# Performance work log

Measured on AMD Instinct MI355X. Metric: run time of the kernel, lower is better.

## Reference

```python
import jax, jax.numpy as jnp
import numpy as np

N_NODES = 100000
DROPOUT_P = 0.2


def _gcn_conv(x, W, b, src, dst, n_nodes):
    # PyG GCNConv: h = x @ W; add self-loops; sym-norm deg^-1/2 aggregation; + bias
    h = x @ W  # [N, D_out]
    loops = jnp.arange(n_nodes, dtype=src.dtype)
    src_all = jnp.concatenate([src, loops])
    dst_all = jnp.concatenate([dst, loops])
    deg = jax.ops.segment_sum(jnp.ones_like(dst_all, dtype=h.dtype), dst_all,
                              num_segments=n_nodes)  # includes self-loops
    dinv = jnp.where(deg > 0, jax.lax.rsqrt(deg), 0.0)
    norm = dinv[src_all] * dinv[dst_all]  # [E+N]
    msg = h[src_all] * norm[:, None]      # gather + scale
    out = jax.ops.segment_sum(msg, dst_all, num_segments=n_nodes)  # scatter-add
    return out + b


def setup_inputs() -> dict:
    key = jax.random.key(0)
    k1, k2, k3, k4 = jax.random.split(key, 4)
    x = jax.random.normal(k1, (N_NODES, 128), dtype=jnp.float32)
    edge_index = jax.random.randint(k2, (2, 1600000), 0, N_NODES, dtype=jnp.int64)
    W1 = jax.random.normal(k3, (128, 64), dtype=jnp.float32) * (1.0 / np.sqrt(128))
    b1 = jnp.zeros((64,), dtype=jnp.float32)
    W2 = jax.random.normal(k4, (64, 32), dtype=jnp.float32) * (1.0 / np.sqrt(64))
    b2 = jnp.zeros((32,), dtype=jnp.float32)
    return {"x": x, "edge_index": edge_index, "W1": W1, "b1": b1, "W2": W2, "b2": b2}


def reference(x, edge_index, W1, b1, W2, b2):
    src, dst = edge_index[0], edge_index[1]
    h1 = _gcn_conv(x, W1, b1, src, dst, N_NODES)
    h1 = jax.nn.relu(h1)
    # F.dropout defaults to training=True -> apply inverted dropout with fixed key
    keep = jax.random.bernoulli(jax.random.key(42), 1.0 - DROPOUT_P, h1.shape)
    h1 = jnp.where(keep, h1 / (1.0 - DROPOUT_P), 0.0)
    h2 = _gcn_conv(h1, W2, b2, src, dst, N_NODES)
    return h2
```

## Files before the change

kernel.cpp:

```cpp
#include <hip/hip_runtime.h>
#include <stdint.h>

#define DIN 128
#define D1 64
#define D2 32
#define MAXDEG 48
#define BCAP 4608
#define CBLK 2048

__device__ __forceinline__ unsigned short f2bf(float v) {
  unsigned u = __float_as_uint(v);
  unsigned r = u + 0x7fffu + ((u >> 16) & 1u);
  return (unsigned short)(r >> 16);
}
__device__ __forceinline__ float bflo(unsigned u) { return __uint_as_float(u << 16); }
__device__ __forceinline__ float bfhi(unsigned u) { return __uint_as_float(u & 0xffff0000u); }

__device__ __forceinline__ unsigned rotl32(unsigned x, int r) {
  return (x << r) | (x >> (32 - r));
}

__device__ __forceinline__ unsigned threefry_fold(unsigned ctr) {
  unsigned k0 = 0u, k1 = 42u;
  unsigned ks0 = k0, ks1 = k1, ks2 = k0 ^ k1 ^ 0x1BD11BDAu;
  unsigned x0 = 0u, x1 = ctr;
  x0 += ks0; x1 += ks1;
#define TF_ROUND(r) { x0 += x1; x1 = rotl32(x1, (r)); x1 ^= x0; }
  TF_ROUND(13) TF_ROUND(15) TF_ROUND(26) TF_ROUND(6)
  x0 += ks1; x1 += ks2 + 1u;
  TF_ROUND(17) TF_ROUND(29) TF_ROUND(16) TF_ROUND(24)
  x0 += ks2; x1 += ks0 + 2u;
  TF_ROUND(13) TF_ROUND(15) TF_ROUND(26) TF_ROUND(6)
  x0 += ks0; x1 += ks1 + 3u;
  TF_ROUND(17) TF_ROUND(29) TF_ROUND(16) TF_ROUND(24)
  x0 += ks1; x1 += ks2 + 4u;
  TF_ROUND(13) TF_ROUND(15) TF_ROUND(26) TF_ROUND(6)
  x0 += ks2; x1 += ks0 + 5u;
#undef TF_ROUND
  return x0 ^ x1;
}

__device__ __forceinline__ float dropout_scale(unsigned idx) {
  unsigned bits = threefry_fold(idx);
  float u = __uint_as_float((bits >> 9) | 0x3f800000u) - 1.0f;
  return (u < 0.8f) ? 1.25f : 0.0f;
}

__device__ __forceinline__ uint4 grow64(const unsigned short* p, int s, int fc) {
  return *(const uint4*)((const char*)p + (((unsigned)s << 7) + ((unsigned)fc << 1)));
}
__device__ __forceinline__ uint4 grow32(const unsigned short* p, int s, int fc) {
  return *(const uint4*)((const char*)p + (((unsigned)s << 6) + ((unsigned)fc << 1)));
}

__device__ __forceinline__ void addpk(float2& a, unsigned u) {
  a.x += bflo(u);
  a.y += bfhi(u);
}
__device__ __forceinline__ void addpkm(float2& a, unsigned u, float m) {
  a.x = fmaf(m, bflo(u), a.x);
  a.y = fmaf(m, bfhi(u), a.y);
}

__global__ __launch_bounds__(256) void bin_kernel(const int* __restrict__ src,
                                                  const int* __restrict__ dst,
                                                  int* __restrict__ cursor,
                                                  uint2* __restrict__ binned,
                                                  int E, int NBK) {
  __shared__ int cnt[512];
  __shared__ int cbase[512];
  const int tid = threadIdx.x;
  const int e0 = blockIdx.x * CBLK;

  for (int b = tid; b < NBK; b += 256) cnt[b] = 0;
  __syncthreads();

#pragma unroll
  for (int i = 0; i < CBLK / 256; i++) {
    int e = e0 + tid + 256 * i;
    if (e < E) atomicAdd(&cnt[dst[e] >> 8], 1);
  }
  __syncthreads();

  for (int b = tid; b < NBK; b += 256) {
    int c = cnt[b];
    if (c > 0) cbase[b] = b * BCAP + atomicAdd(&cursor[b], c);
    cnt[b] = 0;
  }
  __syncthreads();

#pragma unroll
  for (int i = 0; i < CBLK / 256; i++) {
    int e = e0 + tid + 256 * i;
    if (e < E) {
      int d = dst[e];
      int b = d >> 8;
      int rk = atomicAdd(&cnt[b], 1);
      int pos = cbase[b] + rk;
      if (pos - b * BCAP < BCAP)
        binned[pos] = make_uint2((unsigned)d, (unsigned)src[e]);
    }
  }
}

__global__ __launch_bounds__(256) void ellbuild_kernel(const uint2* __restrict__ binned,
                                                       const int* __restrict__ cursor,
                                                       int* __restrict__ deg,
                                                       float* __restrict__ dinv,
                                                       int* __restrict__ ell, int N) {
  __shared__ int r[256];
  const int tid = threadIdx.x;
  const int b = blockIdx.x;
  const int nodebase = b << 8;
  r[tid] = 0;
  __syncthreads();

  int cnt = cursor[b];
  if (cnt > BCAP) cnt = BCAP;
  const uint2* seg = binned + (size_t)b * BCAP;
  for (int i = tid; i < cnt; i += 256) {
    uint2 p = seg[i];
    int local = (int)p.x - nodebase;
    int rk = atomicAdd(&r[local], 1);
    if (rk < MAXDEG) ell[(int)p.x * MAXDEG + rk] = (int)p.y;
  }
  __syncthreads();

  int node = nodebase + tid;
  if (node < N) {
    int dg = r[tid];
    deg[node] = dg;
    dinv[node] = (float)(1.0 / sqrt((double)(dg + 1)));
  }
}

__global__ __launch_bounds__(256) void gemm1_kernel(const float* __restrict__ x,
                                                    const float* __restrict__ W1,
                                                    const float* __restrict__ dinv,
                                                    unsigned short* __restrict__ h1p, int N) {
  __shared__ float xT[32][65];
  __shared__ float Wl[32][D1];
  const int tid = threadIdx.x;
  const int rowbase = blockIdx.x * 64;
  const int tx = tid & 15;
  const int ty = tid >> 4;
  float acc[4][4];
#pragma unroll
  for (int i = 0; i < 4; i++)
#pragma unroll
    for (int j = 0; j < 4; j++) acc[i][j] = 0.f;

  for (int c4 = 0; c4 < 4; c4++) {
    const int k0 = c4 * 32;
#pragma unroll
    for (int i = 0; i < 2; i++) {
      int f = tid + 256 * i;
      int row = f >> 3;
      int kq = (f & 7) * 4;
      int gr = rowbase + row;
      float4 vv = make_float4(0.f, 0.f, 0.f, 0.f);
      if (gr < N) vv = *(const float4*)(x + (size_t)gr * DIN + k0 + kq);
      xT[kq + 0][row] = vv.x;
      xT[kq + 1][row] = vv.y;
      xT[kq + 2][row] = vv.z;
      xT[kq + 3][row] = vv.w;
    }
#pragma unroll
    for (int i = 0; i < 2; i++) {
      int f = tid + 256 * i;
      int k = f >> 4;
      int cc = (f & 15) * 4;
      *(float4*)&Wl[k][cc] = *(const float4*)(W1 + (size_t)(k0 + k) * D1 + cc);
    }
    __syncthreads();
#pragma unroll 4
    for (int k = 0; k < 32; k++) {
      float4 a = *(const float4*)&xT[k][4 * ty];
      float4 b = *(const float4*)&Wl[k][4 * tx];
      float av[4] = {a.x, a.y, a.z, a.w};
      float bv[4] = {b.x, b.y, b.z, b.w};
#pragma unroll
      for (int i = 0; i < 4; i++)
#pragma unroll
        for (int j = 0; j < 4; j++) acc[i][j] = fmaf(av[i], bv[j], acc[i][j]);
    }
    __syncthreads();
  }

#pragma unroll
  for (int i = 0; i < 4; i++) {
    int gr = rowbase + 4 * ty + i;
    if (gr < N) {
      float di = dinv[gr];
      ushort4 o;
      o.x = f2bf(acc[i][0] * di);
      o.y = f2bf(acc[i][1] * di);
      o.z = f2bf(acc[i][2] * di);
      o.w = f2bf(acc[i][3] * di);
      *(ushort4*)(h1p + (size_t)gr * D1 + 4 * tx) = o;
    }
  }
}

__global__ __launch_bounds__(256) void agg1_kernel(const int* __restrict__ deg,
                                                   const float* __restrict__ dinv,
                                                   const int* __restrict__ ell,
                                                   const unsigned short* __restrict__ h1p,
                                                   const float* __restrict__ b1,
                                                   float* __restrict__ h1d, int N) {
  __shared__ float red[4][528];
  const int wslot = __builtin_amdgcn_readfirstlane(threadIdx.x >> 6);
  const int d = blockIdx.x * 4 + wslot;
  const int lane = threadIdx.x & 63;
  const int eslot = lane >> 3;
  const int fc = (lane & 7) << 3;
  const int cnt = min(deg[d], MAXDEG);
  const int base = d * MAXDEG;

  float2 acc[4];
  {
    uint4 sv = grow64(h1p, d, fc);
    float m = (eslot == 0) ? 1.0f : 0.0f;
    acc[0] = make_float2(m * bflo(sv.x), m * bfhi(sv.x));
    acc[1] = make_float2(m * bflo(sv.y), m * bfhi(sv.y));
    acc[2] = make_float2(m * bflo(sv.z), m * bfhi(sv.z));
    acc[3] = make_float2(m * bflo(sv.w), m * bfhi(sv.w));
  }

  int j = 0;
  for (; j + 16 <= cnt; j += 16) {
    int s0 = ell[base + j + eslot];
    int s1 = ell[base + j + 8 + eslot];
    uint4 v0 = grow64(h1p, s0, fc);
    uint4 v1 = grow64(h1p, s1, fc);
    addpk(acc[0], v0.x); addpk(acc[1], v0.y); addpk(acc[2], v0.z); addpk(acc[3], v0.w);
    addpk(acc[0], v1.x); addpk(acc[1], v1.y); addpk(acc[2], v1.z); addpk(acc[3], v1.w);
  }
  if (j < cnt) {
    int e0 = j + eslot;
    int e1 = e0 + 8;
    int s0 = ell[base + e0];
    int s1 = ell[base + e1];
    s0 = (e0 < cnt) ? s0 : d;
    s1 = (e1 < cnt) ? s1 : d;
    float m0 = (e0 < cnt) ? 1.0f : 0.0f;
    float m1 = (e1 < cnt) ? 1.0f : 0.0f;
    uint4 v0 = grow64(h1p, s0, fc);
    uint4 v1 = grow64(h1p, s1, fc);
    addpkm(acc[0], v0.x, m0); addpkm(acc[1], v0.y, m0); addpkm(acc[2], v0.z, m0); addpkm(acc[3], v0.w, m0);
    addpkm(acc[0], v1.x, m1); addpkm(acc[1], v1.y, m1); addpkm(acc[2], v1.z, m1); addpkm(acc[3], v1.w, m1);
  }

  float* wred = red[wslot];
  *(float4*)&wred[eslot * 66 + fc]     = make_float4(acc[0].x, acc[0].y, acc[1].x, acc[1].y);
  *(float4*)&wred[eslot * 66 + fc + 4] = make_float4(acc[2].x, acc[2].y, acc[3].x, acc[3].y);
  const int f = fc + eslot;
  float v = 0.f;
#pragma unroll
  for (int e = 0; e < 8; e++) v += wred[e * 66 + f];

  float o = fmaf(dinv[d], v, b1[f]);
  o = fmaxf(o, 0.0f);
  o *= dropout_scale((unsigned)(d * D1 + f));
  h1d[(size_t)d * D1 + f] = o;
}

__global__ __launch_bounds__(256) void gemm2_kernel(const float* __restrict__ h1d,
                                                    const float* __restrict__ W2,
                                                    const float* __restrict__ dinv,
                                                    unsigned short* __restrict__ h2p, int N) {
  __shared__ float hT[D1][129];
  __shared__ float Wl[D1][D2];
  const int tid = threadIdx.x;
  const int rowbase = blockIdx.x * 128;

#pragma unroll
  for (int i = 0; i < 8; i++) {
    int f = tid + 256 * i;
    int row = f >> 4;
    int kq = (f & 15) * 4;
    int gr = rowbase + row;
    float4 v = make_float4(0.f, 0.f, 0.f, 0.f);
    if (gr < N) v = *(const float4*)(h1d + (size_t)gr * D1 + kq);
    hT[kq + 0][row] = v.x;
    hT[kq + 1][row] = v.y;
    hT[kq + 2][row] = v.z;
    hT[kq + 3][row] = v.w;
  }
#pragma unroll
  for (int i = 0; i < 2; i++) {
    int f = tid + 256 * i;
    int k = f >> 3;
    int c = (f & 7) * 4;
    *(float4*)&Wl[k][c] = *(const float4*)(W2 + (size_t)k * D2 + c);
  }
  __syncthreads();

  const int tx = tid & 7;
  const int ty = tid >> 3;
  float acc[4][4];
#pragma unroll
  for (int i = 0; i < 4; i++)
#pragma unroll
    for (int j = 0; j < 4; j++) acc[i][j] = 0.f;

#pragma unroll 4
  for (int k = 0; k < D1; k++) {
    float4 a = *(const float4*)&hT[k][4 * ty];
    float4 b = *(const float4*)&Wl[k][4 * tx];
    float av[4] = {a.x, a.y, a.z, a.w};
    float bv[4] = {b.x, b.y, b.z, b.w};
#pragma unroll
    for (int i = 0; i < 4; i++)
#pragma unroll
      for (int j = 0; j < 4; j++) acc[i][j] = fmaf(av[i], bv[j], acc[i][j]);
  }

#pragma unroll
  for (int i = 0; i < 4; i++) {
    int gr = rowbase + 4 * ty + i;
    if (gr < N) {
      float di = dinv[gr];
      ushort4 o;
      o.x = f2bf(acc[i][0] * di);
      o.y = f2bf(acc[i][1] * di);
      o.z = f2bf(acc[i][2] * di);
      o.w = f2bf(acc[i][3] * di);
      *(ushort4*)(h2p + (size_t)gr * D2 + 4 * tx) = o;
    }
  }
}

__global__ __launch_bounds__(256) void agg2_kernel(const int* __restrict__ deg,
                                                   const float* __restrict__ dinv,
                                                   const int* __restrict__ ell,
                                                   const unsigned short* __restrict__ h2p,
                                                   const float* __restrict__ b2,
                                                   float* __restrict__ out, int N) {
  __shared__ float red[4][544];
  const int wslot = __builtin_amdgcn_readfirstlane(threadIdx.x >> 6);
  const int d = blockIdx.x * 4 + wslot;
  const int lane = threadIdx.x & 63;
  const int eslot = lane >> 2;
  const int fc = (lane & 3) << 3;
  const int cnt = min(deg[d], MAXDEG);
  const int base = d * MAXDEG;

  float2 acc[4];
  {
    uint4 sv = grow32(h2p, d, fc);
    float m = (eslot == 0) ? 1.0f : 0.0f;
    acc[0] = make_float2(m * bflo(sv.x), m * bfhi(sv.x));
    acc[1] = make_float2(m * bflo(sv.y), m * bfhi(sv.y));
    acc[2] = make_float2(m * bflo(sv.z), m * bfhi(sv.z));
    acc[3] = make_float2(m * bflo(sv.w), m * bfhi(sv.w));
  }

  int j = 0;
  for (; j + 16 <= cnt; j += 16) {
    int s = ell[base + j + eslot];
    uint4 v = grow32(h2p, s, fc);
    addpk(acc[0], v.x); addpk(acc[1], v.y); addpk(acc[2], v.z); addpk(acc[3], v.w);
  }
  if (j < cnt) {
    int e = j + eslot;
    int s = ell[base + e];
    s = (e < cnt) ? s : d;
    float m = (e < cnt) ? 1.0f : 0.0f;
    uint4 v = grow32(h2p, s, fc);
    addpkm(acc[0], v.x, m); addpkm(acc[1], v.y, m); addpkm(acc[2], v.z, m); addpkm(acc[3], v.w, m);
  }

  float* wred = red[wslot];
  *(float4*)&wred[eslot * 34 + fc]     = make_float4(acc[0].x, acc[0].y, acc[1].x, acc[1].y);
  *(float4*)&wred[eslot * 34 + fc + 4] = make_float4(acc[2].x, acc[2].y, acc[3].x, acc[3].y);
  const int f = fc + (eslot & 7);
  const int ebase = (lane >= 32) ? 8 : 0;
  float v = 0.f;
#pragma unroll
  for (int e = 0; e < 8; e++) v += wred[(ebase + e) * 34 + f];
  v += __shfl_down(v, 32, 64);

  if (lane < 32) {
    out[(size_t)d * D2 + f] = fmaf(dinv[d], v, b2[f]);
  }
}

extern "C" void kernel_launch(void* const* d_in, const int* in_sizes, int n_in,
                              void* d_out, int out_size, void* d_ws, size_t ws_size,
                              hipStream_t stream) {
  const float* x  = (const float*)d_in[0];
  const int*   ei = (const int*)d_in[1];
  const float* W1 = (const float*)d_in[2];
  const float* b1 = (const float*)d_in[3];
  const float* W2 = (const float*)d_in[4];
  const float* b2 = (const float*)d_in[5];
  const int N = in_sizes[0] / DIN;
  const int E = in_sizes[1] / 2;
  const int NBK = (N + 255) >> 8;
  const int* src = ei;
  const int* dst = ei + E;
  float* out = (float*)d_out;

  char* ws = (char*)d_ws;
  size_t off = 0;
  auto alloc = [&](size_t bytes) -> char* {
    char* p = ws + off;
    off += (bytes + 255) / 256 * 256;
    return p;
  };
  unsigned short* h1p = (unsigned short*)alloc((size_t)N * D1 * 2);
  float*          h1d = (float*)alloc((size_t)N * D1 * 4);
  int*            ell = (int*)alloc(((size_t)N * MAXDEG + 64) * 4);
  int*            deg = (int*)alloc((size_t)N * 4);
  float*        dinvp = (float*)alloc((size_t)N * 4);
  int*         cursor = (int*)alloc((size_t)NBK * 4);
  unsigned short* h2p = h1p;
  uint2*       binned = (uint2*)h1d;
  (void)ws_size; (void)n_in; (void)out_size;

  hipMemsetAsync(cursor, 0, (size_t)NBK * 4, stream);

  bin_kernel<<<(E + CBLK - 1) / CBLK, 256, 0, stream>>>(src, dst, cursor, binned, E, NBK);
  ellbuild_kernel<<<NBK, 256, 0, stream>>>(binned, cursor, deg, dinvp, ell, N);
  gemm1_kernel<<<(N + 63) / 64, 256, 0, stream>>>(x, W1, dinvp, h1p, N);
  agg1_kernel<<<N / 4, 256, 0, stream>>>(deg, dinvp, ell, h1p, b1, h1d, N);
  gemm2_kernel<<<(N + 127) / 128, 256, 0, stream>>>(h1d, W2, dinvp, h2p, N);
  agg2_kernel<<<N / 4, 256, 0, stream>>>(deg, dinvp, ell, h2p, b2, out, N);
}
```

Measured before the change: 262.3 us.

## Replace shared-memory binning with sub-bucketed global atomics; fully unroll neighbor gathers

The binning kernel drops the per-block shared-memory histogram and two-pass scatter. Each edge now does a single global atomic into one of 16 sub-buckets per 256-node bucket, chosen by block index to spread contention, and ellbuild walks all 16 sub-buckets. Both aggregation kernels load the whole 48-entry ELL row with one coalesced load per lane and broadcast indices by shuffle. They then issue all gathers up front, fully unrolled and masked, instead of looping. This removes the dependent index loads and exposes more memory parallelism, at the cost of always issuing MAXDEG gathers and more global atomic traffic. Sub-buckets can overflow at SUBCAP 384 more easily than the old single 4608 cap.

```diff
diff --git a/kernel.cpp b/kernel.cpp
--- a/kernel.cpp
+++ b/kernel.cpp
@@ -5,8 +5,8 @@
 #define D1 64
 #define D2 32
 #define MAXDEG 48
-#define BCAP 4608
-#define CBLK 2048
+#define SUBC 16
+#define SUBCAP 384
 
 __device__ __forceinline__ unsigned short f2bf(float v) {
   unsigned u = __float_as_uint(v);
@@ -53,10 +53,6 @@
   return *(const uint4*)((const char*)p + (((unsigned)s << 6) + ((unsigned)fc << 1)));
 }
 
-__device__ __forceinline__ void addpk(float2& a, unsigned u) {
-  a.x += bflo(u);
-  a.y += bfhi(u);
-}
 __device__ __forceinline__ void addpkm(float2& a, unsigned u, float m) {
   a.x = fmaf(m, bflo(u), a.x);
   a.y = fmaf(m, bfhi(u), a.y);
@@ -65,42 +61,15 @@
 __global__ __launch_bounds__(256) void bin_kernel(const int* __restrict__ src,
                                                   const int* __restrict__ dst,
                                                   int* __restrict__ cursor,
-                                                  uint2* __restrict__ binned,
-                                                  int E, int NBK) {
-  __shared__ int cnt[512];
-  __shared__ int cbase[512];
-  const int tid = threadIdx.x;
-  const int e0 = blockIdx.x * CBLK;
-
-  for (int b = tid; b < NBK; b += 256) cnt[b] = 0;
-  __syncthreads();
-
-#pragma unroll
-  for (int i = 0; i < CBLK / 256; i++) {
-    int e = e0 + tid + 256 * i;
-    if (e < E) atomicAdd(&cnt[dst[e] >> 8], 1);
-  }
-  __syncthreads();
-
-  for (int b = tid; b < NBK; b += 256) {
-    int c = cnt[b];
-    if (c > 0) cbase[b] = b * BCAP + atomicAdd(&cursor[b], c);
-    cnt[b] = 0;
-  }
-  __syncthreads();
-
-#pragma unroll
-  for (int i = 0; i < CBLK / 256; i++) {
-    int e = e0 + tid + 256 * i;
-    if (e < E) {
-      int d = dst[e];
-      int b = d >> 8;
-      int rk = atomicAdd(&cnt[b], 1);
-      int pos = cbase[b] + rk;
-      if (pos - b * BCAP < BCAP)
-        binned[pos] = make_uint2((unsigned)d, (unsigned)src[e]);
-    }
-  }
+                                                  uint2* __restrict__ binned, int E) {
+  int e = blockIdx.x * 256 + threadIdx.x;
+  if (e >= E) return;
+  int d = dst[e];
+  int s = src[e];
+  int sub = ((d >> 8) << 4) + (blockIdx.x & (SUBC - 1));
+  int rk = atomicAdd(&cursor[sub], 1);
+  if (rk < SUBCAP)
+    binned[(size_t)sub * SUBCAP + rk] = make_uint2((unsigned)d, (unsigned)s);
 }
 
 __global__ __launch_bounds__(256) void ellbuild_kernel(const uint2* __restrict__ binned,
@@ -115,14 +84,17 @@
   r[tid] = 0;
   __syncthreads();
 
-  int cnt = cursor[b];
-  if (cnt > BCAP) cnt = BCAP;
-  const uint2* seg = binned + (size_t)b * BCAP;
-  for (int i = tid; i < cnt; i += 256) {
-    uint2 p = seg[i];
-    int local = (int)p.x - nodebase;
-    int rk = atomicAdd(&r[local], 1);
-    if (rk < MAXDEG) ell[(int)p.x * MAXDEG + rk] = (int)p.y;
+  for (int k = 0; k < SUBC; k++) {
+    int idx = (b << 4) + k;
+    int cnt = cursor[idx];
+    if (cnt > SUBCAP) cnt = SUBCAP;
+    const uint2* seg = binned + (size_t)idx * SUBCAP;
+    for (int i = tid; i < cnt; i += 256) {
+      uint2 p = seg[i];
+      int local = (int)p.x - nodebase;
+      int rk = atomicAdd(&r[local], 1);
+      if (rk < MAXDEG) ell[(int)p.x * MAXDEG + rk] = (int)p.y;
+    }
   }
   __syncthreads();
 
@@ -217,49 +189,45 @@
   const int cnt = min(deg[d], MAXDEG);
   const int base = d * MAXDEG;
 
+  int sv = ell[base + lane];
+
+  uint4 v[6];
+  float mk[6];
+#pragma unroll
+  for (int seg = 0; seg < 6; seg++) {
+    int e = seg * 8 + eslot;
+    int s = __shfl(sv, e, 64);
+    bool ok = e < cnt;
+    mk[seg] = ok ? 1.0f : 0.0f;
+    v[seg] = grow64(h1p, ok ? s : d, fc);
+  }
+  uint4 self = grow64(h1p, d, fc);
+
   float2 acc[4];
   {
-    uint4 sv = grow64(h1p, d, fc);
     float m = (eslot == 0) ? 1.0f : 0.0f;
-    acc[0] = make_float2(m * bflo(sv.x), m * bfhi(sv.x));
-    acc[1] = make_float2(m * bflo(sv.y), m * bfhi(sv.y));
-    acc[2] = make_float2(m * bflo(sv.z), m * bfhi(sv.z));
-    acc[3] = make_float2(m * bflo(sv.w), m * bfhi(sv.w));
-  }
-
-  int j = 0;
-  for (; j + 16 <= cnt; j += 16) {
-    int s0 = ell[base + j + eslot];
-    int s1 = ell[base + j + 8 + eslot];
-    uint4 v0 = grow64(h1p, s0, fc);
-    uint4 v1 = grow64(h1p, s1, fc);
-    addpk(acc[0], v0.x); addpk(acc[1], v0.y); addpk(acc[2], v0.z); addpk(acc[3], v0.w);
-    addpk(acc[0], v1.x); addpk(acc[1], v1.y); addpk(acc[2], v1.z); addpk(acc[3], v1.w);
-  }
-  if (j < cnt) {
-    int e0 = j + eslot;
-    int e1 = e0 + 8;
-    int s0 = ell[base + e0];
-    int s1 = ell[base + e1];
-    s0 = (e0 < cnt) ? s0 : d;
-    s1 = (e1 < cnt) ? s1 : d;
-    float m0 = (e0 < cnt) ? 1.0f : 0.0f;
-    float m1 = (e1 < cnt) ? 1.0f : 0.0f;
-    uint4 v0 = grow64(h1p, s0, fc);
-    uint4 v1 = grow64(h1p, s1, fc);
-    addpkm(acc[0], v0.x, m0); addpkm(acc[1], v0.y, m0); addpkm(acc[2], v0.z, m0); addpkm(acc[3], v0.w, m0);
-    addpkm(acc[0], v1.x, m1); addpkm(acc[1], v1.y, m1); addpkm(acc[2], v1.z, m1); addpkm(acc[3], v1.w, m1);
+    acc[0] = make_float2(m * bflo(self.x), m * bfhi(self.x));
+    acc[1] = make_float2(m * bflo(self.y), m * bfhi(self.y));
+    acc[2] = make_float2(m * bflo(self.z), m * bfhi(self.z));
+    acc[3] = make_float2(m * bflo(self.w), m * bfhi(self.w));
+  }
+#pragma unroll
+  for (int seg = 0; seg < 6; seg++) {
+    addpkm(acc[0], v[seg].x, mk[seg]);
+    addpkm(acc[1], v[seg].y, mk[seg]);
+    addpkm(acc[2], v[seg].z, mk[seg]);
+    addpkm(acc[3], v[seg].w, mk[seg]);
   }
 
   float* wred = red[wslot];
   *(float4*)&wred[eslot * 66 + fc]     = make_float4(acc[0].x, acc[0].y, acc[1].x, acc[1].y);
   *(float4*)&wred[eslot * 66 + fc + 4] = make_float4(acc[2].x, acc[2].y, acc[3].x, acc[3].y);
   const int f = fc + eslot;
-  float v = 0.f;
-#pragma unroll
-  for (int e = 0; e < 8; e++) v += wred[e * 66 + f];
-
-  float o = fmaf(dinv[d], v, b1[f]);
+  float vsum = 0.f;
+#pragma unroll
+  for (int e = 0; e < 8; e++) vsum += wred[e * 66 + f];
+
+  float o = fmaf(dinv[d], vsum, b1[f]);
   o = fmaxf(o, 0.0f);
   o *= dropout_scale((unsigned)(d * D1 + f));
   h1d[(size_t)d * D1 + f] = o;
@@ -346,29 +314,34 @@
   const int cnt = min(deg[d], MAXDEG);
   const int base = d * MAXDEG;
 
+  int sv = ell[base + lane];
+
+  uint4 v[3];
+  float mk[3];
+#pragma unroll
+  for (int seg = 0; seg < 3; seg++) {
+    int e = seg * 16 + eslot;
+    int s = __shfl(sv, e, 64);
+    bool ok = e < cnt;
+    mk[seg] = ok ? 1.0f : 0.0f;
+    v[seg] = grow32(h2p, ok ? s : d, fc);
+  }
+  uint4 self = grow32(h2p, d, fc);
+
   float2 acc[4];
   {
-    uint4 sv = grow32(h2p, d, fc);
     float m = (eslot == 0) ? 1.0f : 0.0f;
-    acc[0] = make_float2(m * bflo(sv.x), m * bfhi(sv.x));
-    acc[1] = make_float2(m * bflo(sv.y), m * bfhi(sv.y));
-    acc[2] = make_float2(m * bflo(sv.z), m * bfhi(sv.z));
-    acc[3] = make_float2(m * bflo(sv.w), m * bfhi(sv.w));
-  }
-
-  int j = 0;
-  for (; j + 16 <= cnt; j += 16) {
-    int s = ell[base + j + eslot];
-    uint4 v = grow32(h2p, s, fc);
-    addpk(acc[0], v.x); addpk(acc[1], v.y); addpk(acc[2], v.z); addpk(acc[3], v.w);
-  }
-  if (j < cnt) {
-    int e = j + eslot;
-    int s = ell[base + e];
-    s = (e < cnt) ? s : d;
-    float m = (e < cnt) ? 1.0f : 0.0f;
-    uint4 v = grow32(h2p, s, fc);
-    addpkm(acc[0], v.x, m); addpkm(acc[1], v.y, m); addpkm(acc[2], v.z, m); addpkm(acc[3], v.w, m);
+    acc[0] = make_float2(m * bflo(self.x), m * bfhi(self.x));
+    acc[1] = make_float2(m * bflo(self.y), m * bfhi(self.y));
+    acc[2] = make_float2(m * bflo(self.z), m * bfhi(self.z));
+    acc[3] = make_float2(m * bflo(self.w), m * bfhi(self.w));
+  }
+#pragma unroll
+  for (int seg = 0; seg < 3; seg++) {
+    addpkm(acc[0], v[seg].x, mk[seg]);
+    addpkm(acc[1], v[seg].y, mk[seg]);
+    addpkm(acc[2], v[seg].z, mk[seg]);
+    addpkm(acc[3], v[seg].w, mk[seg]);
   }
 
   float* wred = red[wslot];
@@ -376,13 +349,13 @@
   *(float4*)&wred[eslot * 34 + fc + 4] = make_float4(acc[2].x, acc[2].y, acc[3].x, acc[3].y);
   const int f = fc + (eslot & 7);
   const int ebase = (lane >= 32) ? 8 : 0;
-  float v = 0.f;
-#pragma unroll
-  for (int e = 0; e < 8; e++) v += wred[(ebase + e) * 34 + f];
-  v += __shfl_down(v, 32, 64);
+  float vsum = 0.f;
+#pragma unroll
+  for (int e = 0; e < 8; e++) vsum += wred[(ebase + e) * 34 + f];
+  vsum += __shfl_down(vsum, 32, 64);
 
   if (lane < 32) {
-    out[(size_t)d * D2 + f] = fmaf(dinv[d], v, b2[f]);
+    out[(size_t)d * D2 + f] = fmaf(dinv[d], vsum, b2[f]);
   }
 }
 
@@ -398,6 +371,7 @@
   const int N = in_sizes[0] / DIN;
   const int E = in_sizes[1] / 2;
   const int NBK = (N + 255) >> 8;
+  const int NSUB = NBK * SUBC;
   const int* src = ei;
   const int* dst = ei + E;
   float* out = (float*)d_out;
@@ -414,14 +388,14 @@
   int*            ell = (int*)alloc(((size_t)N * MAXDEG + 64) * 4);
   int*            deg = (int*)alloc((size_t)N * 4);
   float*        dinvp = (float*)alloc((size_t)N * 4);
-  int*         cursor = (int*)alloc((size_t)NBK * 4);
+  int*         cursor = (int*)alloc((size_t)NSUB * 4);
   unsigned short* h2p = h1p;
   uint2*       binned = (uint2*)h1d;
   (void)ws_size; (void)n_in; (void)out_size;
 
-  hipMemsetAsync(cursor, 0, (size_t)NBK * 4, stream);
-
-  bin_kernel<<<(E + CBLK - 1) / CBLK, 256, 0, stream>>>(src, dst, cursor, binned, E, NBK);
+  hipMemsetAsync(cursor, 0, (size_t)NSUB * 4, stream);
+
+  bin_kernel<<<(E + 255) / 256, 256, 0, stream>>>(src, dst, cursor, binned, E);
   ellbuild_kernel<<<NBK, 256, 0, stream>>>(binned, cursor, deg, dinvp, ell, N);
   gemm1_kernel<<<(N + 63) / 64, 256, 0, stream>>>(x, W1, dinvp, h1p, N);
   agg1_kernel<<<N / 4, 256, 0, stream>>>(deg, dinvp, ell, h1p, b1, h1d, N);
```

Result: slower. 313.5 us (+19.5%).

## Preload ELL row per wave, issue all neighbor gathers up front, enlarge bin chunks

Applied to the files above, without the earlier changes.

The aggregation kernels now load a node's whole ELL row with one coalesced per-lane read and hand indices out with shuffles. A switch on degree picks a fully unrolled template, so every neighbor row gather is in flight before any accumulation starts, instead of a serial loop of dependent loads. The self row, dinv, bias and dropout scale are also loaded early. The binning kernel processes larger edge chunks (CBLK 2048 to 8192) and caches dst values in shared memory so the second pass skips the global reread. The cost is higher register pressure from the unrolled gathers and more LDS per bin block, which can lower occupancy.

```diff
diff --git a/kernel.cpp b/kernel.cpp
--- a/kernel.cpp
+++ b/kernel.cpp
@@ -6,7 +6,7 @@
 #define D2 32
 #define MAXDEG 48
 #define BCAP 4608
-#define CBLK 2048
+#define CBLK 8192
 
 __device__ __forceinline__ unsigned short f2bf(float v) {
   unsigned u = __float_as_uint(v);
@@ -62,6 +62,56 @@
   a.y = fmaf(m, bfhi(u), a.y);
 }
 
+template <int K>
+__device__ __forceinline__ void gather_acc1(float2 (&acc)[4], int sv, int cnt, int d, int fc,
+                                            const unsigned short* __restrict__ h1p, int eslot) {
+  uint4 v[K];
+#pragma unroll
+  for (int seg = 0; seg < K - 1; seg++) {
+    int s = __shfl(sv, seg * 8 + eslot, 64);
+    v[seg] = grow64(h1p, s, fc);
+  }
+  const int elast = (K - 1) * 8 + eslot;
+  const bool ok = elast < cnt;
+  {
+    int s = __shfl(sv, elast, 64);
+    v[K - 1] = grow64(h1p, ok ? s : d, fc);
+  }
+#pragma unroll
+  for (int seg = 0; seg < K - 1; seg++) {
+    addpk(acc[0], v[seg].x); addpk(acc[1], v[seg].y);
+    addpk(acc[2], v[seg].z); addpk(acc[3], v[seg].w);
+  }
+  const float m = ok ? 1.0f : 0.0f;
+  addpkm(acc[0], v[K - 1].x, m); addpkm(acc[1], v[K - 1].y, m);
+  addpkm(acc[2], v[K - 1].z, m); addpkm(acc[3], v[K - 1].w, m);
+}
+
+template <int K>
+__device__ __forceinline__ void gather_acc2(float2 (&acc)[4], int sv, int cnt, int d, int fc,
+                                            const unsigned short* __restrict__ h2p, int eslot) {
+  uint4 v[K];
+#pragma unroll
+  for (int seg = 0; seg < K - 1; seg++) {
+    int s = __shfl(sv, seg * 16 + eslot, 64);
+    v[seg] = grow32(h2p, s, fc);
+  }
+  const int elast = (K - 1) * 16 + eslot;
+  const bool ok = elast < cnt;
+  {
+    int s = __shfl(sv, elast, 64);
+    v[K - 1] = grow32(h2p, ok ? s : d, fc);
+  }
+#pragma unroll
+  for (int seg = 0; seg < K - 1; seg++) {
+    addpk(acc[0], v[seg].x); addpk(acc[1], v[seg].y);
+    addpk(acc[2], v[seg].z); addpk(acc[3], v[seg].w);
+  }
+  const float m = ok ? 1.0f : 0.0f;
+  addpkm(acc[0], v[K - 1].x, m); addpkm(acc[1], v[K - 1].y, m);
+  addpkm(acc[2], v[K - 1].z, m); addpkm(acc[3], v[K - 1].w, m);
+}
+
 __global__ __launch_bounds__(256) void bin_kernel(const int* __restrict__ src,
                                                   const int* __restrict__ dst,
                                                   int* __restrict__ cursor,
@@ -69,16 +119,19 @@
                                                   int E, int NBK) {
   __shared__ int cnt[512];
   __shared__ int cbase[512];
+  __shared__ int dstbuf[CBLK];
   const int tid = threadIdx.x;
   const int e0 = blockIdx.x * CBLK;
 
   for (int b = tid; b < NBK; b += 256) cnt[b] = 0;
   __syncthreads();
 
-#pragma unroll
+#pragma unroll 4
   for (int i = 0; i < CBLK / 256; i++) {
     int e = e0 + tid + 256 * i;
-    if (e < E) atomicAdd(&cnt[dst[e] >> 8], 1);
+    int dv = (e < E) ? dst[e] : -1;
+    dstbuf[tid + 256 * i] = dv;
+    if (dv >= 0) atomicAdd(&cnt[dv >> 8], 1);
   }
   __syncthreads();
 
@@ -89,11 +142,11 @@
   }
   __syncthreads();
 
-#pragma unroll
+#pragma unroll 4
   for (int i = 0; i < CBLK / 256; i++) {
     int e = e0 + tid + 256 * i;
-    if (e < E) {
-      int d = dst[e];
+    int d = dstbuf[tid + 256 * i];
+    if (d >= 0) {
       int b = d >> 8;
       int rk = atomicAdd(&cnt[b], 1);
       int pos = cbase[b] + rk;
@@ -216,52 +269,43 @@
   const int fc = (lane & 7) << 3;
   const int cnt = min(deg[d], MAXDEG);
   const int base = d * MAXDEG;
+  const int f = fc + eslot;
+
+  int sv = ell[base + lane];
+  uint4 self = grow64(h1p, d, fc);
+  const float di = dinv[d];
+  const float bias = b1[f];
+  const float drop = dropout_scale((unsigned)(d * D1 + f));
 
   float2 acc[4];
   {
-    uint4 sv = grow64(h1p, d, fc);
     float m = (eslot == 0) ? 1.0f : 0.0f;
-    acc[0] = make_float2(m * bflo(sv.x), m * bfhi(sv.x));
-    acc[1] = make_float2(m * bflo(sv.y), m * bfhi(sv.y));
-    acc[2] = make_float2(m * bflo(sv.z), m * bfhi(sv.z));
-    acc[3] = make_float2(m * bflo(sv.w), m * bfhi(sv.w));
-  }
-
-  int j = 0;
-  for (; j + 16 <= cnt; j += 16) {
-    int s0 = ell[base + j + eslot];
-    int s1 = ell[base + j + 8 + eslot];
-    uint4 v0 = grow64(h1p, s0, fc);
-    uint4 v1 = grow64(h1p, s1, fc);
-    addpk(acc[0], v0.x); addpk(acc[1], v0.y); addpk(acc[2], v0.z); addpk(acc[3], v0.w);
-    addpk(acc[0], v1.x); addpk(acc[1], v1.y); addpk(acc[2], v1.z); addpk(acc[3], v1.w);
-  }
-  if (j < cnt) {
-    int e0 = j + eslot;
-    int e1 = e0 + 8;
-    int s0 = ell[base + e0];
-    int s1 = ell[base + e1];
-    s0 = (e0 < cnt) ? s0 : d;
-    s1 = (e1 < cnt) ? s1 : d;
-    float m0 = (e0 < cnt) ? 1.0f : 0.0f;
-    float m1 = (e1 < cnt) ? 1.0f : 0.0f;
-    uint4 v0 = grow64(h1p, s0, fc);
-    uint4 v1 = grow64(h1p, s1, fc);
-    addpkm(acc[0], v0.x, m0); addpkm(acc[1], v0.y, m0); addpkm(acc[2], v0.z, m0); addpkm(acc[3], v0.w, m0);
-    addpkm(acc[0], v1.x, m1); addpkm(acc[1], v1.y, m1); addpkm(acc[2], v1.z, m1); addpkm(acc[3], v1.w, m1);
+    acc[0] = make_float2(m * bflo(self.x), m * bfhi(self.x));
+    acc[1] = make_float2(m * bflo(self.y), m * bfhi(self.y));
+    acc[2] = make_float2(m * bflo(self.z), m * bfhi(self.z));
+    acc[3] = make_float2(m * bflo(self.w), m * bfhi(self.w));
+  }
+
+  switch ((cnt + 7) >> 3) {
+    case 6: gather_acc1<6>(acc, sv, cnt, d, fc, h1p, eslot); break;
+    case 5: gather_acc1<5>(acc, sv, cnt, d, fc, h1p, eslot); break;
+    case 4: gather_acc1<4>(acc, sv, cnt, d, fc, h1p, eslot); break;
+    case 3: gather_acc1<3>(acc, sv, cnt, d, fc, h1p, eslot); break;
+    case 2: gather_acc1<2>(acc, sv, cnt, d, fc, h1p, eslot); break;
+    case 1: gather_acc1<1>(acc, sv, cnt, d, fc, h1p, eslot); break;
+    default: break;
   }
 
   float* wred = red[wslot];
   *(float4*)&wred[eslot * 66 + fc]     = make_float4(acc[0].x, acc[0].y, acc[1].x, acc[1].y);
   *(float4*)&wred[eslot * 66 + fc + 4] = make_float4(acc[2].x, acc[2].y, acc[3].x, acc[3].y);
-  const int f = fc + eslot;
-  float v = 0.f;
-#pragma unroll
-  for (int e = 0; e < 8; e++) v += wred[e * 66 + f];
-
-  float o = fmaf(dinv[d], v, b1[f]);
+  float vsum = 0.f;
+#pragma unroll
+  for (int e = 0; e < 8; e++) vsum += wred[e * 66 + f];
+
+  float o = fmaf(di, vsum, bias);
   o = fmaxf(o, 0.0f);
-  o *= dropout_scale((unsigned)(d * D1 + f));
+  o *= drop;
   h1d[(size_t)d * D1 + f] = o;
 }
 
@@ -346,29 +390,24 @@
   const int cnt = min(deg[d], MAXDEG);
   const int base = d * MAXDEG;
 
+  int sv = ell[base + lane];
+  uint4 self = grow32(h2p, d, fc);
+  const float di = dinv[d];
+
   float2 acc[4];
   {
-    uint4 sv = grow32(h2p, d, fc);
     float m = (eslot == 0) ? 1.0f : 0.0f;
-    acc[0] = make_float2(m * bflo(sv.x), m * bfhi(sv.x));
-    acc[1] = make_float2(m * bflo(sv.y), m * bfhi(sv.y));
-    acc[2] = make_float2(m * bflo(sv.z), m * bfhi(sv.z));
-    acc[3] = make_float2(m * bflo(sv.w), m * bfhi(sv.w));
-  }
-
-  int j = 0;
-  for (; j + 16 <= cnt; j += 16) {
-    int s = ell[base + j + eslot];
-    uint4 v = grow32(h2p, s, fc);
-    addpk(acc[0], v.x); addpk(acc[1], v.y); addpk(acc[2], v.z); addpk(acc[3], v.w);
-  }
-  if (j < cnt) {
-    int e = j + eslot;
-    int s = ell[base + e];
-    s = (e < cnt) ? s : d;
-    float m = (e < cnt) ? 1.0f : 0.0f;
-    uint4 v = grow32(h2p, s, fc);
-    addpkm(acc[0], v.x, m); addpkm(acc[1], v.y, m); addpkm(acc[2], v.z, m); addpkm(acc[3], v.w, m);
+    acc[0] = make_float2(m * bflo(self.x), m * bfhi(self.x));
+    acc[1] = make_float2(m * bflo(self.y), m * bfhi(self.y));
+    acc[2] = make_float2(m * bflo(self.z), m * bfhi(self.z));
+    acc[3] = make_float2(m * bflo(self.w), m * bfhi(self.w));
+  }
+
+  switch ((cnt + 15) >> 4) {
+    case 3: gather_acc2<3>(acc, sv, cnt, d, fc, h2p, eslot); break;
+    case 2: gather_acc2<2>(acc, sv, cnt, d, fc, h2p, eslot); break;
+    case 1: gather_acc2<1>(acc, sv, cnt, d, fc, h2p, eslot); break;
+    default: break;
   }
 
   float* wred = red[wslot];
@@ -376,13 +415,13 @@
   *(float4*)&wred[eslot * 34 + fc + 4] = make_float4(acc[2].x, acc[2].y, acc[3].x, acc[3].y);
   const int f = fc + (eslot & 7);
   const int ebase = (lane >= 32) ? 8 : 0;
-  float v = 0.f;
-#pragma unroll
-  for (int e = 0; e < 8; e++) v += wred[(ebase + e) * 34 + f];
-  v += __shfl_down(v, 32, 64);
+  float vsum = 0.f;
+#pragma unroll
+  for (int e = 0; e < 8; e++) vsum += wred[(ebase + e) * 34 + f];
+  vsum += __shfl_down(vsum, 32, 64);
 
   if (lane < 32) {
-    out[(size_t)d * D2 + f] = fmaf(dinv[d], v, b2[f]);
+    out[(size_t)d * D2 + f] = fmaf(di, vsum, b2[f]);
   }
 }
 
```

After: 245.4 us. -6.4%, faster.
